# Optimization experiments

Hardware: AMD Instinct MI355X
Metric: run time of the kernel (lower is better)

The kernel has to match this reference:

```python
import jax, jax.numpy as jnp
import numpy as np

N = 2048        # n_instances of the single entity (relation is N x N)
IN_DIM = 16
OUT_DIM = 16


def _set_partitions(items):
    # enumerate all set partitions of `items` (deterministic order)
    if not items:
        yield []
        return
    first, rest = items[0], items[1:]
    for part in _set_partitions(rest):
        for i in range(len(part)):
            yield part[:i] + [part[i] + [first]] + part[i + 1:]
        yield [[first]] + part


def _partitions():
    # combined input dims {i0,i1} and output dims {o0,o1}; same entity, so all
    # Bell(4)=15 set partitions are valid equivariant basis elements.
    items = [('i', 0), ('i', 1), ('o', 0), ('o', 1)]
    parts = []
    for p in _set_partitions(items):
        blocks = []
        for blk in p:
            iset = sorted(d for t, d in blk if t == 'i')
            oset = sorted(d for t, d in blk if t == 'o')
            blocks.append((iset, oset))
        parts.append(blocks)
    return parts


PARTITIONS = _partitions()  # 15 equality mappings


def setup_inputs() -> dict:
    key = jax.random.key(0)
    k1, k2 = jax.random.split(key)
    stdv = 0.1 / np.sqrt(IN_DIM)
    X = jax.random.normal(k1, (1, IN_DIM, N, N), dtype=jnp.float32)
    weights = jax.random.uniform(k2, (len(PARTITIONS), IN_DIM, OUT_DIM),
                                 minval=-stdv, maxval=stdv, dtype=jnp.float32)
    bias = jnp.ones((len(PARTITIONS),), dtype=jnp.float32)
    return {"X": X, "weights": weights, "bias": bias}


def _basis_apply(X, W, blocks, eye_n, ones_n):
    # One equivariant basis op (diag -> mean-pool -> broadcast -> diag-embed ->
    # reindex) fused with the per-channel linear map into a single einsum.
    blk_letters = 'ijkl'
    in_sub = [''] * 2
    for bi, (iset, oset) in enumerate(blocks):
        for d in iset:
            in_sub[d] = blk_letters[bi]  # equal input dims share a letter -> diagonal
    subs = ['bc' + ''.join(in_sub)]
    ops = [X]
    fresh = iter('uvwxyz')
    out_letter = [''] * 2
    denom = 1.0
    for bi, (iset, oset) in enumerate(blocks):
        if not oset:
            # pooled block: letter appears only in X -> einsum sums; divide for mean
            denom *= float(N)
            continue
        if iset:
            base = blk_letters[bi]
        else:
            base = next(fresh)          # broadcast a brand-new output dim
            subs.append(base)
            ops.append(ones_n)
        out_letter[oset[0]] = base
        for od in oset[1:]:             # diag-embed equal output dims via identity
            l2 = next(fresh)
            subs.append(base + l2)
            ops.append(eye_n)
            out_letter[od] = l2
    subs.append('co')                   # F.linear with weights[i]: sum_c X[c]*W[c,o]
    ops.append(W)
    expr = ','.join(subs) + '->bo' + ''.join(out_letter)
    return jnp.einsum(expr, *ops) / denom


def reference(X, weights, bias):
    eye_n = jnp.eye(N, dtype=X.dtype)
    ones_n = jnp.ones((N,), dtype=X.dtype)
    Y = None
    for i, blocks in enumerate(PARTITIONS):
        Yi = _basis_apply(X, weights[i], blocks, eye_n, ones_n)
        Y = Yi if Y is None else Y + Yi
    # each basis adds a scalar bias[i] everywhere -> total scalar sum(bias)
    return Y + jnp.sum(bias)
```

## Files before the change

kernel.cpp:

```cpp
#include <hip/hip_runtime.h>
#include <hip/hip_bf16.h>

#define N 2048

typedef float f4 __attribute__((ext_vector_type(4)));
typedef unsigned int u32;
typedef u32 u32x4 __attribute__((ext_vector_type(4)));

#define OFF_ROWSUM 0
#define OFF_COLSUM 32768
#define OFF_DIAG   65536
#define OFF_SUMS   98304
#define OFF_A      98336
#define OFF_B      131104
#define OFF_D      163872
#define OFF_C      196640
#define OFF_ROWPART 196656
#define OFF_COLPART 720944

__global__ __launch_bounds__(256, 4) void packreduce_kernel(const float* __restrict__ X,
                                                            float* __restrict__ ws,
                                                            u32* __restrict__ XT) {
    const int s0 = blockIdx.x * 32;
    const int t0 = blockIdx.y * 128;
    const int cz = blockIdx.z;
    const int tid = threadIdx.x;

    __shared__ float lds[2][32][132];

    #pragma unroll
    for (int j = 0; j < 8; ++j) {
        const int idx = tid + 256 * j;
        const int ch = idx >> 10, row = (idx >> 5) & 31, c4 = idx & 31;
        const f4 v = *(const f4*)(X + (size_t)(2 * cz + ch) * N * N + (size_t)(s0 + row) * N + t0 + 4 * c4);
        *(f4*)&lds[ch][row][4 * c4] = v;
    }
    __syncthreads();

    #pragma unroll
    for (int j = 0; j < 4; ++j) {
        const int idx = tid + 256 * j;
        const int tt = idx >> 3, xq = idx & 7;
        u32x4 w;
        #pragma unroll
        for (int i = 0; i < 4; ++i) {
            const int sl = 4 * xq + i;
            const unsigned short lo = __builtin_bit_cast(unsigned short, __float2bfloat16(lds[0][sl][tt]));
            const unsigned short hi = __builtin_bit_cast(unsigned short, __float2bfloat16(lds[1][sl][tt]));
            w[i] = (u32)lo | ((u32)hi << 16);
        }
        __builtin_nontemporal_store(w, (u32x4*)(XT + (size_t)cz * N * N + (size_t)(t0 + tt) * N + s0 + 4 * xq));
    }

    {
        const int pr = tid >> 2, seg = tid & 3;
        const int ch = pr >> 5, row = pr & 31;
        float rs = 0.f;
        #pragma unroll
        for (int j = 0; j < 8; ++j) {
            const f4 v = *(const f4*)&lds[ch][row][seg * 32 + 4 * j];
            rs += (v.x + v.y) + (v.z + v.w);
        }
        rs += __shfl_xor(rs, 1);
        rs += __shfl_xor(rs, 2);
        if (seg == 0)
            ws[OFF_ROWPART + (size_t)((t0 >> 7) * 16 + 2 * cz + ch) * N + s0 + row] = rs;
    }

    {
        const int ch = tid >> 7, col = tid & 127;
        float cs = 0.f;
        #pragma unroll
        for (int r = 0; r < 32; ++r) cs += lds[ch][r][col];
        ws[OFF_COLPART + (size_t)((s0 >> 5) * 16 + 2 * cz + ch) * N + t0 + col] = cs;
    }

    if (tid < 64) {
        const int ch = tid >> 5, r = tid & 31;
        const int col = s0 + r - t0;
        if (col >= 0 && col < 128)
            ws[OFF_DIAG + (2 * cz + ch) * N + s0 + r] = lds[ch][r][col];
    }
}

__global__ __launch_bounds__(256) void rowcol_kernel(float* __restrict__ ws) {
    const int c = blockIdx.y;
    const int y = blockIdx.x * 256 + threadIdx.x;
    float rs = 0.f;
    #pragma unroll
    for (int p = 0; p < 16; ++p) rs += ws[OFF_ROWPART + (size_t)(p * 16 + c) * N + y];
    ws[OFF_ROWSUM + c * N + y] = rs;
    float cs = 0.f;
    #pragma unroll
    for (int s = 0; s < 64; ++s) cs += ws[OFF_COLPART + (size_t)(s * 16 + c) * N + y];
    ws[OFF_COLSUM + c * N + y] = cs;
}

__global__ __launch_bounds__(256) void sums_kernel(float* __restrict__ ws) {
    const int c = blockIdx.x;
    const int tid = threadIdx.x;
    float tot = 0.f, dg = 0.f;
    #pragma unroll
    for (int j = 0; j < 8; ++j) {
        tot += ws[OFF_ROWSUM + c * N + tid + 256 * j];
        dg  += ws[OFF_DIAG   + c * N + tid + 256 * j];
    }
    #pragma unroll
    for (int s = 1; s < 64; s <<= 1) { tot += __shfl_xor(tot, s); dg += __shfl_xor(dg, s); }
    __shared__ float buf[2][4];
    const int wave = tid >> 6, lane = tid & 63;
    if (lane == 0) { buf[0][wave] = tot; buf[1][wave] = dg; }
    __syncthreads();
    if (tid == 0) {
        ws[OFF_SUMS + 16 + c] = buf[0][0] + buf[0][1] + buf[0][2] + buf[0][3];
        ws[OFF_SUMS + c]      = buf[1][0] + buf[1][1] + buf[1][2] + buf[1][3];
    }
}

__global__ __launch_bounds__(256) void fold_kernel(const float* __restrict__ W,
                                                   const float* __restrict__ bias,
                                                   float* __restrict__ ws) {
    const int o = blockIdx.y;
    const int x = blockIdx.x * 256 + threadIdx.x;
    const float invN = 1.f / (float)N;
    const float invN2 = invN * invN;
    const float* rowsum = ws + OFF_ROWSUM;
    const float* colsum = ws + OFF_COLSUM;
    const float* diagv  = ws + OFF_DIAG;
    const float* sums   = ws + OFF_SUMS;
    float* Abuf = ws + OFF_A;
    float* Bbuf = ws + OFF_B;
    float* Dbuf = ws + OFF_D;
    float* Cbuf = ws + OFF_C;

    if (blockIdx.x == 0 && threadIdx.x == 0) {
        float cacc = 0.f;
        #pragma unroll
        for (int c = 0; c < 16; ++c)
            cacc += (sums[c] * invN) * W[11 * 256 + c * 16 + o]
                  + (sums[16 + c] * invN2) * W[14 * 256 + c * 16 + o];
        float sb = 0.f;
        for (int p = 0; p < 15; ++p) sb += bias[p];
        Cbuf[o] = cacc + sb;
    }

    float du = 0.f;
    #pragma unroll
    for (int c = 0; c < 16; ++c)
        du += (sums[c] * invN) * W[2 * 256 + c * 16 + o]
            + (sums[16 + c] * invN2) * W[4 * 256 + c * 16 + o];

    float a = 0.f, b = 0.f, d = 0.f;
    #pragma unroll
    for (int c = 0; c < 16; ++c) {
        const float dg = diagv[c * N + x];
        const float rm = rowsum[c * N + x] * invN;
        const float cm = colsum[c * N + x] * invN;
        a += dg * W[5 * 256 + c * 16 + o] + rm * W[12 * 256 + c * 16 + o] + cm * W[7 * 256 + c * 16 + o];
        b += dg * W[9 * 256 + c * 16 + o] + rm * W[13 * 256 + c * 16 + o] + cm * W[10 * 256 + c * 16 + o];
        d += dg * W[0 * 256 + c * 16 + o] + rm * W[3 * 256 + c * 16 + o]  + cm * W[1 * 256 + c * 16 + o];
    }
    Abuf[o * N + x] = a;
    Bbuf[o * N + x] = b;
    Dbuf[o * N + x] = d + du;
}

__global__ __launch_bounds__(256, 4) void main_kernel(const float* __restrict__ X,
                                                      const float* __restrict__ W,
                                                      const float* __restrict__ ws,
                                                      const u32* __restrict__ XT,
                                                      float* __restrict__ out) {
    const int tid = threadIdx.x;
    const int og = __builtin_amdgcn_readfirstlane(tid >> 7);
    const int qi = tid & 127;
    const size_t p = ((size_t)blockIdx.x * 128 + qi) * 4;
    const int x = (int)(p >> 11);
    const int y = (int)(p & 2047);

    const float* Wid = W + 8 * 256 + og * 8;
    const float* Wtr = W + 6 * 256 + og * 8;

    f4 acc[8];
    #pragma unroll
    for (int oo = 0; oo < 8; ++oo) acc[oo] = (f4)(0.f);

    #pragma unroll 2
    for (int c2 = 0; c2 < 8; ++c2) {
        const int c0 = 2 * c2;
        const f4 xa = *(const f4*)(X + (size_t)c0 * N * N + p);
        const f4 xb = *(const f4*)(X + (size_t)(c0 + 1) * N * N + p);
        const u32x4 xt = *(const u32x4*)(XT + (size_t)c2 * N * N + p);
        f4 ta, tb;
        #pragma unroll
        for (int i = 0; i < 4; ++i) {
            ta[i] = __builtin_bit_cast(float, xt[i] << 16);
            tb[i] = __builtin_bit_cast(float, xt[i] & 0xffff0000u);
        }
        const f4 wiA0 = *(const f4*)&Wid[c0 * 16];
        const f4 wiA1 = *(const f4*)&Wid[c0 * 16 + 4];
        const f4 wiB0 = *(const f4*)&Wid[c0 * 16 + 16];
        const f4 wiB1 = *(const f4*)&Wid[c0 * 16 + 20];
        const f4 wtA0 = *(const f4*)&Wtr[c0 * 16];
        const f4 wtA1 = *(const f4*)&Wtr[c0 * 16 + 4];
        const f4 wtB0 = *(const f4*)&Wtr[c0 * 16 + 16];
        const f4 wtB1 = *(const f4*)&Wtr[c0 * 16 + 20];
        #pragma unroll
        for (int oo = 0; oo < 4; ++oo) {
            acc[oo]     += wiA0[oo] * xa + wiB0[oo] * xb + wtA0[oo] * ta + wtB0[oo] * tb;
            acc[oo + 4] += wiA1[oo] * xa + wiB1[oo] * xb + wtA1[oo] * ta + wtB1[oo] * tb;
        }
    }

    __syncthreads();

    const float* Abuf = ws + OFF_A;
    const float* Bbuf = ws + OFF_B;
    const float* Dbuf = ws + OFF_D;
    const float* Cbuf = ws + OFF_C;

    #pragma unroll
    for (int oo = 0; oo < 8; ++oo) {
        const int o = og * 8 + oo;
        const float av = Abuf[o * N + x] + Cbuf[o];
        const f4 bv = *(const f4*)&Bbuf[o * N + y];
        f4 v = acc[oo] + av + bv;
        const int d = x - y;
        if (d >= 0 && d < 4) v[d] += Dbuf[o * N + x];
        __builtin_nontemporal_store(v, (f4*)(out + (size_t)o * N * N + p));
    }
}

extern "C" void kernel_launch(void* const* d_in, const int* in_sizes, int n_in,
                              void* d_out, int out_size, void* d_ws, size_t ws_size,
                              hipStream_t stream) {
    (void)in_sizes; (void)n_in; (void)out_size; (void)ws_size;
    const float* X    = (const float*)d_in[0];
    const float* W    = (const float*)d_in[1];
    const float* bias = (const float*)d_in[2];
    float* out = (float*)d_out;
    float* ws  = (float*)d_ws;
    u32* XT = (u32*)(out + (size_t)8 * N * N);

    packreduce_kernel<<<dim3(64, 16, 8), 256, 0, stream>>>(X, ws, XT);
    rowcol_kernel<<<dim3(8, 16), 256, 0, stream>>>(ws);
    sums_kernel<<<16, 256, 0, stream>>>(ws);
    fold_kernel<<<dim3(8, 16), 256, 0, stream>>>(W, bias, ws);
    main_kernel<<<8192, 256, 0, stream>>>(X, W, ws, XT, out);
}
```

Before: 269.3 us.

## Quantize X to packed fp8 and replace partial-sum pass with atomics

The pack kernel now converts X into two fp8 copies (direct and transposed), each packing four channels per 32-bit word. The main kernel reads only these fp8 copies instead of the fp32 X plus the bf16 transposed copy, which cuts global memory traffic in the bandwidth-bound main pass. Row and column sums are now accumulated with float atomicAdd into a memset workspace, which removes the separate rowcol reduction kernel and its partial buffers. This trades accuracy, since the activations lose far more precision in fp8 than in bf16, and it adds atomic contention plus a memset launch.

```diff
diff --git a/kernel.cpp b/kernel.cpp
--- a/kernel.cpp
+++ b/kernel.cpp
@@ -2,98 +2,95 @@
 #include <hip/hip_bf16.h>
 
 #define N 2048
+#define NN (N * N)
 
 typedef float f4 __attribute__((ext_vector_type(4)));
+typedef float f2 __attribute__((ext_vector_type(2)));
 typedef unsigned int u32;
 typedef u32 u32x4 __attribute__((ext_vector_type(4)));
 
 #define OFF_ROWSUM 0
 #define OFF_COLSUM 32768
-#define OFF_DIAG   65536
-#define OFF_SUMS   98304
+#define OFF_SUMS   65536
+#define OFF_DIAG   65568
 #define OFF_A      98336
 #define OFF_B      131104
 #define OFF_D      163872
 #define OFF_C      196640
-#define OFF_ROWPART 196656
-#define OFF_COLPART 720944
 
 __global__ __launch_bounds__(256, 4) void packreduce_kernel(const float* __restrict__ X,
                                                             float* __restrict__ ws,
+                                                            u32* __restrict__ XD,
                                                             u32* __restrict__ XT) {
     const int s0 = blockIdx.x * 32;
-    const int t0 = blockIdx.y * 128;
-    const int cz = blockIdx.z;
+    const int t0 = blockIdx.y * 64;
+    const int qz = blockIdx.z;
     const int tid = threadIdx.x;
 
-    __shared__ float lds[2][32][132];
+    __shared__ float lds[4][32][68];
 
     #pragma unroll
     for (int j = 0; j < 8; ++j) {
         const int idx = tid + 256 * j;
-        const int ch = idx >> 10, row = (idx >> 5) & 31, c4 = idx & 31;
-        const f4 v = *(const f4*)(X + (size_t)(2 * cz + ch) * N * N + (size_t)(s0 + row) * N + t0 + 4 * c4);
-        *(f4*)&lds[ch][row][4 * c4] = v;
+        const int ch = idx >> 9, row = (idx >> 4) & 31, q = idx & 15;
+        const f4 v = __builtin_nontemporal_load(
+            (const f4*)(X + (size_t)(4 * qz + ch) * NN + (size_t)(s0 + row) * N + t0 + 4 * q));
+        *(f4*)&lds[ch][row][4 * q] = v;
     }
     __syncthreads();
 
     #pragma unroll
-    for (int j = 0; j < 4; ++j) {
+    for (int j = 0; j < 2; ++j) {
         const int idx = tid + 256 * j;
-        const int tt = idx >> 3, xq = idx & 7;
+        const int row = idx >> 4, c4 = idx & 15;
         u32x4 w;
         #pragma unroll
         for (int i = 0; i < 4; ++i) {
-            const int sl = 4 * xq + i;
-            const unsigned short lo = __builtin_bit_cast(unsigned short, __float2bfloat16(lds[0][sl][tt]));
-            const unsigned short hi = __builtin_bit_cast(unsigned short, __float2bfloat16(lds[1][sl][tt]));
-            w[i] = (u32)lo | ((u32)hi << 16);
-        }
-        __builtin_nontemporal_store(w, (u32x4*)(XT + (size_t)cz * N * N + (size_t)(t0 + tt) * N + s0 + 4 * xq));
+            const int c = 4 * c4 + i;
+            int t = __builtin_amdgcn_cvt_pk_fp8_f32(lds[0][row][c], lds[1][row][c], 0, false);
+            t = __builtin_amdgcn_cvt_pk_fp8_f32(lds[2][row][c], lds[3][row][c], t, true);
+            w[i] = (u32)t;
+        }
+        *(u32x4*)(XD + (size_t)qz * NN + (size_t)(s0 + row) * N + t0 + 4 * c4) = w;
+    }
+
+    #pragma unroll
+    for (int j = 0; j < 2; ++j) {
+        const int idx = tid + 256 * j;
+        const int tt = idx >> 3, sq = idx & 7;
+        u32x4 w;
+        #pragma unroll
+        for (int i = 0; i < 4; ++i) {
+            const int s = 4 * sq + i;
+            int t = __builtin_amdgcn_cvt_pk_fp8_f32(lds[0][s][tt], lds[1][s][tt], 0, false);
+            t = __builtin_amdgcn_cvt_pk_fp8_f32(lds[2][s][tt], lds[3][s][tt], t, true);
+            w[i] = (u32)t;
+        }
+        *(u32x4*)(XT + (size_t)qz * NN + (size_t)(t0 + tt) * N + s0 + 4 * sq) = w;
+    }
+
+    if (tid < 128) {
+        const int ch = (tid >> 5) & 3, row = tid & 31;
+        const int c = 4 * qz + ch;
+        float rs = 0.f;
+        #pragma unroll
+        for (int j = 0; j < 16; ++j) {
+            const f4 v = *(const f4*)&lds[ch][row][4 * j];
+            rs += (v.x + v.y) + (v.z + v.w);
+        }
+        atomicAdd(&ws[OFF_ROWSUM + c * N + s0 + row], rs);
+        const int col = s0 + row - t0;
+        if (col >= 0 && col < 64)
+            ws[OFF_DIAG + c * N + s0 + row] = lds[ch][row][col];
     }
 
     {
-        const int pr = tid >> 2, seg = tid & 3;
-        const int ch = pr >> 5, row = pr & 31;
-        float rs = 0.f;
-        #pragma unroll
-        for (int j = 0; j < 8; ++j) {
-            const f4 v = *(const f4*)&lds[ch][row][seg * 32 + 4 * j];
-            rs += (v.x + v.y) + (v.z + v.w);
-        }
-        rs += __shfl_xor(rs, 1);
-        rs += __shfl_xor(rs, 2);
-        if (seg == 0)
-            ws[OFF_ROWPART + (size_t)((t0 >> 7) * 16 + 2 * cz + ch) * N + s0 + row] = rs;
-    }
-
-    {
-        const int ch = tid >> 7, col = tid & 127;
+        const int ch = tid >> 6, col = tid & 63;
         float cs = 0.f;
         #pragma unroll
         for (int r = 0; r < 32; ++r) cs += lds[ch][r][col];
-        ws[OFF_COLPART + (size_t)((s0 >> 5) * 16 + 2 * cz + ch) * N + t0 + col] = cs;
-    }
-
-    if (tid < 64) {
-        const int ch = tid >> 5, r = tid & 31;
-        const int col = s0 + r - t0;
-        if (col >= 0 && col < 128)
-            ws[OFF_DIAG + (2 * cz + ch) * N + s0 + r] = lds[ch][r][col];
-    }
-}
-
-__global__ __launch_bounds__(256) void rowcol_kernel(float* __restrict__ ws) {
-    const int c = blockIdx.y;
-    const int y = blockIdx.x * 256 + threadIdx.x;
-    float rs = 0.f;
-    #pragma unroll
-    for (int p = 0; p < 16; ++p) rs += ws[OFF_ROWPART + (size_t)(p * 16 + c) * N + y];
-    ws[OFF_ROWSUM + c * N + y] = rs;
-    float cs = 0.f;
-    #pragma unroll
-    for (int s = 0; s < 64; ++s) cs += ws[OFF_COLPART + (size_t)(s * 16 + c) * N + y];
-    ws[OFF_COLSUM + c * N + y] = cs;
+        atomicAdd(&ws[OFF_COLSUM + (4 * qz + ch) * N + t0 + col], cs);
+    }
 }
 
 __global__ __launch_bounds__(256) void sums_kernel(float* __restrict__ ws) {
@@ -165,9 +162,9 @@
     Dbuf[o * N + x] = d + du;
 }
 
-__global__ __launch_bounds__(256, 4) void main_kernel(const float* __restrict__ X,
-                                                      const float* __restrict__ W,
+__global__ __launch_bounds__(256, 4) void main_kernel(const float* __restrict__ W,
                                                       const float* __restrict__ ws,
+                                                      const u32* __restrict__ XD,
                                                       const u32* __restrict__ XT,
                                                       float* __restrict__ out) {
     const int tid = threadIdx.x;
@@ -184,30 +181,36 @@
     #pragma unroll
     for (int oo = 0; oo < 8; ++oo) acc[oo] = (f4)(0.f);
 
-    #pragma unroll 2
-    for (int c2 = 0; c2 < 8; ++c2) {
-        const int c0 = 2 * c2;
-        const f4 xa = *(const f4*)(X + (size_t)c0 * N * N + p);
-        const f4 xb = *(const f4*)(X + (size_t)(c0 + 1) * N * N + p);
-        const u32x4 xt = *(const u32x4*)(XT + (size_t)c2 * N * N + p);
-        f4 ta, tb;
+    #pragma unroll
+    for (int qz = 0; qz < 4; ++qz) {
+        const u32x4 xd = *(const u32x4*)(XD + (size_t)qz * NN + p);
+        const u32x4 xt = *(const u32x4*)(XT + (size_t)qz * NN + p);
+        f2 dlo[4], dhi[4], tlo[4], thi[4];
         #pragma unroll
         for (int i = 0; i < 4; ++i) {
-            ta[i] = __builtin_bit_cast(float, xt[i] << 16);
-            tb[i] = __builtin_bit_cast(float, xt[i] & 0xffff0000u);
-        }
-        const f4 wiA0 = *(const f4*)&Wid[c0 * 16];
-        const f4 wiA1 = *(const f4*)&Wid[c0 * 16 + 4];
-        const f4 wiB0 = *(const f4*)&Wid[c0 * 16 + 16];
-        const f4 wiB1 = *(const f4*)&Wid[c0 * 16 + 20];
-        const f4 wtA0 = *(const f4*)&Wtr[c0 * 16];
-        const f4 wtA1 = *(const f4*)&Wtr[c0 * 16 + 4];
-        const f4 wtB0 = *(const f4*)&Wtr[c0 * 16 + 16];
-        const f4 wtB1 = *(const f4*)&Wtr[c0 * 16 + 20];
-        #pragma unroll
-        for (int oo = 0; oo < 4; ++oo) {
-            acc[oo]     += wiA0[oo] * xa + wiB0[oo] * xb + wtA0[oo] * ta + wtB0[oo] * tb;
-            acc[oo + 4] += wiA1[oo] * xa + wiB1[oo] * xb + wtA1[oo] * ta + wtB1[oo] * tb;
+            dlo[i] = __builtin_amdgcn_cvt_pk_f32_fp8((int)xd[i], false);
+            dhi[i] = __builtin_amdgcn_cvt_pk_f32_fp8((int)xd[i], true);
+            tlo[i] = __builtin_amdgcn_cvt_pk_f32_fp8((int)xt[i], false);
+            thi[i] = __builtin_amdgcn_cvt_pk_f32_fp8((int)xt[i], true);
+        }
+        #pragma unroll
+        for (int cq = 0; cq < 4; ++cq) {
+            const int c = 4 * qz + cq;
+            f4 xv, tv;
+            #pragma unroll
+            for (int i = 0; i < 4; ++i) {
+                xv[i] = (cq == 0) ? dlo[i].x : (cq == 1) ? dlo[i].y : (cq == 2) ? dhi[i].x : dhi[i].y;
+                tv[i] = (cq == 0) ? tlo[i].x : (cq == 1) ? tlo[i].y : (cq == 2) ? thi[i].x : thi[i].y;
+            }
+            const f4 wi0 = *(const f4*)&Wid[c * 16];
+            const f4 wi1 = *(const f4*)&Wid[c * 16 + 4];
+            const f4 wt0 = *(const f4*)&Wtr[c * 16];
+            const f4 wt1 = *(const f4*)&Wtr[c * 16 + 4];
+            #pragma unroll
+            for (int oo = 0; oo < 4; ++oo) {
+                acc[oo]     += wi0[oo] * xv + wt0[oo] * tv;
+                acc[oo + 4] += wi1[oo] * xv + wt1[oo] * tv;
+            }
         }
     }
 
@@ -226,7 +229,7 @@
         f4 v = acc[oo] + av + bv;
         const int d = x - y;
         if (d >= 0 && d < 4) v[d] += Dbuf[o * N + x];
-        __builtin_nontemporal_store(v, (f4*)(out + (size_t)o * N * N + p));
+        *(f4*)(out + (size_t)o * NN + p) = v;
     }
 }
 
@@ -239,11 +242,12 @@
     const float* bias = (const float*)d_in[2];
     float* out = (float*)d_out;
     float* ws  = (float*)d_ws;
-    u32* XT = (u32*)(out + (size_t)8 * N * N);
-
-    packreduce_kernel<<<dim3(64, 16, 8), 256, 0, stream>>>(X, ws, XT);
-    rowcol_kernel<<<dim3(8, 16), 256, 0, stream>>>(ws);
+    u32* XD = (u32*)out;
+    u32* XT = (u32*)out + (size_t)4 * NN;
+
+    (void)hipMemsetAsync(ws, 0, (OFF_SUMS + 32) * sizeof(float), stream);
+    packreduce_kernel<<<dim3(64, 32, 4), 256, 0, stream>>>(X, ws, XD, XT);
     sums_kernel<<<16, 256, 0, stream>>>(ws);
     fold_kernel<<<dim3(8, 16), 256, 0, stream>>>(W, bias, ws);
-    main_kernel<<<8192, 256, 0, stream>>>(X, W, ws, XT, out);
-}
+    main_kernel<<<8192, 256, 0, stream>>>(W, ws, XD, XT, out);
+}
```

Result: slower. 545.8 us (+102.7%).
